# Kernel tuning notes

Hardware: AMD Instinct MI355X
Metric: run time of the kernel (lower is better)

Reference implementation:

```python
import jax, jax.numpy as jnp
import numpy as np

B, S, D, H, F = 8, 1024, 768, 12, 3072
DH = D // H
C_QUAD = 5.0
LN_EPS = 1e-5


def layer_norm(x, g, b):
    mu = jnp.mean(x, axis=-1, keepdims=True)
    var = jnp.mean(jnp.square(x - mu), axis=-1, keepdims=True)
    return (x - mu) * jax.lax.rsqrt(var + LN_EPS) * g + b


def setup_inputs() -> dict:
    key = jax.random.key(0)
    ks = jax.random.split(key, 8)
    s_in = 1.0 / np.sqrt(D)
    s_ff = 1.0 / np.sqrt(F)
    return {
        "x": jax.random.normal(ks[0], (B, S, D), jnp.float32),
        "wqkv": jax.random.normal(ks[1], (D, 3 * D), jnp.float32) * s_in,
        "bqkv": jnp.zeros((3 * D,), jnp.float32),
        "wo": jax.random.normal(ks[2], (D, D), jnp.float32) * s_in,
        "bo": jnp.zeros((D,), jnp.float32),
        "ln1_g": jnp.ones((D,), jnp.float32),
        "ln1_b": jnp.zeros((D,), jnp.float32),
        "w1": jax.random.normal(ks[3], (D, F), jnp.float32) * s_in,
        "b1": jnp.zeros((F,), jnp.float32),
        "w2": jax.random.normal(ks[4], (F, D), jnp.float32) * s_ff,
        "b2": jnp.zeros((D,), jnp.float32),
        "ln2_g": jnp.ones((D,), jnp.float32),
        "ln2_b": jnp.zeros((D,), jnp.float32),
    }


def quad2(scores):
    # Quad2 custom 'softmax': (s + c)^2 normalized by row sum
    s2 = jnp.square(scores + C_QUAD)
    return s2 / jnp.sum(s2, axis=-1, keepdims=True)


def reference(x, wqkv, bqkv, wo, bo, ln1_g, ln1_b, w1, b1, w2, b2, ln2_g, ln2_b):
    # --- pre-norm multi-head attention with Quad2 score normalization ---
    h = layer_norm(x, ln1_g, ln1_b)
    qkv = h @ wqkv + bqkv                              # [B,S,3D]
    q, k, v = jnp.split(qkv, 3, axis=-1)
    q = q.reshape(B, S, H, DH).transpose(0, 2, 1, 3)   # [B,H,S,Dh]
    k = k.reshape(B, S, H, DH).transpose(0, 2, 1, 3)
    v = v.reshape(B, S, H, DH).transpose(0, 2, 1, 3)
    scale = 1.0 / np.sqrt(DH)
    scores = jnp.einsum("bhqd,bhkd->bhqk", q, k) * scale
    attn = quad2(scores)                               # [B,H,S,S]
    ctx = jnp.einsum("bhqk,bhkd->bhqd", attn, v)
    ctx = ctx.transpose(0, 2, 1, 3).reshape(B, S, D)
    x = x + ctx @ wo + bo
    # --- pre-norm FFN ---
    h = layer_norm(x, ln2_g, ln2_b)
    h = jax.nn.gelu(h @ w1 + b1)
    x = x + h @ w2 + b2
    return x
```

## Files before the change

kernel.cpp:

```cpp
#include <hip/hip_runtime.h>
#include <hip/hip_bf16.h>

constexpr int B_ = 8;
constexpr int S_ = 1024;
constexpr int D_ = 768;
constexpr int H_ = 12;
constexpr int F_ = 3072;
constexpr int DH_ = 64;
constexpr int M_ = B_ * S_;
constexpr int PSZ = B_ * S_ * D_;

typedef __bf16 bf16x8 __attribute__((ext_vector_type(8)));
typedef float f32x4 __attribute__((ext_vector_type(4)));
typedef short s16x8 __attribute__((ext_vector_type(8)));
typedef short s16x4 __attribute__((ext_vector_type(4)));

__device__ __forceinline__ void gload_lds16(const __bf16* g, __bf16* l) {
    __builtin_amdgcn_global_load_lds(
        (const __attribute__((address_space(1))) void*)g,
        (__attribute__((address_space(3))) void*)l,
        16, 0, 0);
}

__device__ __forceinline__ float fast_gelu(float x) {
    float x3 = x * x * x;
    float z = 0.7978845608028654f * x + 0.035677408136300125f * x3;
    float e = __builtin_amdgcn_exp2f(-2.8853900817779268f * z);
    return x * __builtin_amdgcn_rcpf(1.0f + e);
}

__global__ __launch_bounds__(256) void transpose_cvt(const float* __restrict__ in,
                                                     __bf16* __restrict__ out,
                                                     int K, int N) {
    __shared__ float t[32][33];
    int tx = threadIdx.x, ty = threadIdx.y;
    int n0 = blockIdx.x * 32, k0 = blockIdx.y * 32;
#pragma unroll
    for (int i = 0; i < 4; ++i)
        t[ty + i * 8][tx] = in[(size_t)(k0 + ty + i * 8) * N + n0 + tx];
    __syncthreads();
#pragma unroll
    for (int i = 0; i < 4; ++i)
        out[(size_t)(n0 + ty + i * 8) * K + k0 + tx] = (__bf16)t[tx][ty + i * 8];
}

__global__ __launch_bounds__(256) void ln_kernel(const float* __restrict__ x,
                                                 const float* __restrict__ g,
                                                 const float* __restrict__ bb,
                                                 __bf16* __restrict__ out) {
    int row = blockIdx.x;
    const float* xr = x + (size_t)row * D_;
    int tid = threadIdx.x;
    float v[3];
    float s = 0.f, s2 = 0.f;
#pragma unroll
    for (int j = 0; j < 3; ++j) {
        v[j] = xr[tid + j * 256];
        s += v[j];
        s2 += v[j] * v[j];
    }
#pragma unroll
    for (int o = 32; o >= 1; o >>= 1) {
        s += __shfl_xor(s, o, 64);
        s2 += __shfl_xor(s2, o, 64);
    }
    __shared__ float red[8];
    int wid = tid >> 6, lane = tid & 63;
    if (lane == 0) { red[wid] = s; red[4 + wid] = s2; }
    __syncthreads();
    s = red[0] + red[1] + red[2] + red[3];
    s2 = red[4] + red[5] + red[6] + red[7];
    float mu = s * (1.0f / D_);
    float var = s2 * (1.0f / D_) - mu * mu;
    float rs = rsqrtf(var + 1e-5f);
    __bf16* orow = out + (size_t)row * D_;
#pragma unroll
    for (int j = 0; j < 3; ++j) {
        int i = tid + j * 256;
        orow[i] = (__bf16)((v[j] - mu) * rs * g[i] + bb[i]);
    }
}

template <int EPI>
__global__ __launch_bounds__(512) void gemmk(const __bf16* __restrict__ A,
                                             const __bf16* __restrict__ Bt,
                                             const float* __restrict__ bias,
                                             const float* __restrict__ res,
                                             float* __restrict__ outf,
                                             __bf16* __restrict__ outb,
                                             int M, int N, int K) {
    __shared__ __bf16 lds[2][16384];

    const int tid = threadIdx.x;
    const int lane = tid & 63, wid = tid >> 6;
    const int wm = wid >> 2, wn = wid & 3;
    const int gx = gridDim.x;
    const int nwg = gx * gridDim.y;
    int flat = blockIdx.y * gx + blockIdx.x;
    flat = (flat & 7) * (nwg >> 3) + (flat >> 3);
    const int bm = (flat / gx) * 128, bn = (flat % gx) * 128;
    const int l15 = lane & 15, l4 = lane >> 4;
    f32x4 acc[4][2] = {};

    const int r8 = tid >> 3;
    const int swc = ((tid & 7) ^ (r8 & 7)) * 8;
    const __bf16* ga = A + (size_t)(bm + r8) * K + swc;
    const __bf16* gb = Bt + (size_t)(bn + r8) * K + swc;
    const int NT = K / 64;

    auto stage = [&](int t, int s) {
        const int kt = t * 64;
        __bf16* base = &lds[s][0] + tid * 8;
        gload_lds16(ga + kt, base);
        gload_lds16(ga + kt + (size_t)64 * K, base + 4096);
        gload_lds16(gb + kt, base + 8192);
        gload_lds16(gb + kt + (size_t)64 * K, base + 12288);
    };

    stage(0, 0);
    for (int t = 0; t < NT; ++t) {
        if (t + 1 < NT) {
            stage(t + 1, (t + 1) & 1);
            asm volatile("s_waitcnt vmcnt(4)" ::: "memory");
        } else {
            asm volatile("s_waitcnt vmcnt(0)" ::: "memory");
        }
        asm volatile("s_barrier" ::: "memory");

        const __bf16* sA = &lds[t & 1][0];
        const __bf16* sB = sA + 8192;
        const int swr = (l15 & 7) * 8;
        bf16x8 a[4][2], b[2][2];
#pragma unroll
        for (int mf = 0; mf < 4; ++mf) {
            int row = wm * 64 + mf * 16 + l15;
#pragma unroll
            for (int ks = 0; ks < 2; ++ks)
                a[mf][ks] = *(const bf16x8*)&sA[row * 64 + ((ks * 32 + l4 * 8) ^ swr)];
        }
#pragma unroll
        for (int nf = 0; nf < 2; ++nf) {
            int row = wn * 32 + nf * 16 + l15;
#pragma unroll
            for (int ks = 0; ks < 2; ++ks)
                b[nf][ks] = *(const bf16x8*)&sB[row * 64 + ((ks * 32 + l4 * 8) ^ swr)];
        }
        asm volatile("s_waitcnt lgkmcnt(0)" ::: "memory");
        asm volatile("s_barrier" ::: "memory");
        __builtin_amdgcn_sched_barrier(0);

        __builtin_amdgcn_s_setprio(1);
#pragma unroll
        for (int ks = 0; ks < 2; ++ks)
#pragma unroll
            for (int mf = 0; mf < 4; ++mf)
#pragma unroll
                for (int nf = 0; nf < 2; ++nf)
                    acc[mf][nf] = __builtin_amdgcn_mfma_f32_16x16x32_bf16(
                        a[mf][ks], b[nf][ks], acc[mf][nf], 0, 0, 0);
        __builtin_amdgcn_s_setprio(0);
    }

    if constexpr (EPI == 0) {
#pragma unroll
        for (int nf = 0; nf < 2; ++nf) {
            int n = bn + wn * 32 + nf * 16 + l15;
            int part = n / 768;
            int n7 = n - part * 768;
            float bv = bias[n];
            size_t obase = (size_t)part * PSZ + (size_t)(n7 >> 6) * (S_ * DH_) + (n7 & 63);
#pragma unroll
            for (int mf = 0; mf < 4; ++mf) {
                int m0 = bm + wm * 64 + mf * 16 + l4 * 4;
                size_t rb = obase + (size_t)(m0 >> 10) * ((size_t)H_ * S_ * DH_) +
                            (size_t)(m0 & 1023) * DH_;
#pragma unroll
                for (int r = 0; r < 4; ++r)
                    outb[rb + (size_t)r * DH_] = (__bf16)(acc[mf][nf][r] + bv);
            }
        }
    } else {
#pragma unroll
        for (int mf = 0; mf < 4; ++mf) {
#pragma unroll
            for (int nf = 0; nf < 2; ++nf) {
#pragma unroll
                for (int r = 0; r < 4; ++r) {
                    int m = bm + wm * 64 + mf * 16 + l4 * 4 + r;
                    int n = bn + wn * 32 + nf * 16 + l15;
                    float val = acc[mf][nf][r] + bias[n];
                    if constexpr (EPI == 1) {
                        outf[(size_t)m * N + n] = val + res[(size_t)m * N + n];
                    } else {
                        outb[(size_t)m * N + n] = (__bf16)fast_gelu(val);
                    }
                }
            }
        }
    }
}

__global__ __launch_bounds__(256) void attn_kernel(const __bf16* __restrict__ qg,
                                                   const __bf16* __restrict__ kg,
                                                   const __bf16* __restrict__ vg,
                                                   __bf16* __restrict__ ctx) {
    __shared__ __bf16 Ks[64][72];
    __shared__ __bf16 Vt[64][72];
    __shared__ __bf16 Pw[4][32][72];
    __shared__ float den_l[4][32];
    int tid = threadIdx.x, lane = tid & 63, wid = tid >> 6;
    int l15 = lane & 15, l4 = lane >> 4;
    int bh = blockIdx.x >> 3, qt = blockIdx.x & 7;
    int q0 = qt * 128;
    const __bf16* qbase = qg + (size_t)bh * S_ * DH_;
    const __bf16* kbase = kg + (size_t)bh * S_ * DH_;
    const __bf16* vbase = vg + (size_t)bh * S_ * DH_;

    int wq0 = q0 + wid * 32;
    bf16x8 qf[2][2];
#pragma unroll
    for (int qi = 0; qi < 2; ++qi)
#pragma unroll
        for (int ks = 0; ks < 2; ++ks)
            qf[qi][ks] = *(const bf16x8*)(qbase + (size_t)(wq0 + qi * 16 + l15) * DH_ +
                                          ks * 32 + l4 * 8);

    f32x4 oacc[2][4] = {};
    float den[2] = {0.f, 0.f};
    const float scale = 0.125f;

    for (int k0 = 0; k0 < S_; k0 += 64) {
        {
            int key = tid >> 2, dc = (tid & 3) * 16;
            *(s16x8*)&Ks[key][dc] =
                *(const s16x8*)(kbase + (size_t)(k0 + key) * DH_ + dc);
            *(s16x8*)&Ks[key][dc + 8] =
                *(const s16x8*)(kbase + (size_t)(k0 + key) * DH_ + dc + 8);
            int vkey = tid & 63, dg = (tid >> 6) * 16;
            s16x8 v0 = *(const s16x8*)(vbase + (size_t)(k0 + vkey) * DH_ + dg);
            s16x8 v1 = *(const s16x8*)(vbase + (size_t)(k0 + vkey) * DH_ + dg + 8);
#pragma unroll
            for (int e = 0; e < 8; ++e) {
                Vt[dg + e][vkey] = ((const __bf16*)&v0)[e];
                Vt[dg + 8 + e][vkey] = ((const __bf16*)&v1)[e];
            }
        }
        __syncthreads();

        bf16x8 kf[4][2];
#pragma unroll
        for (int kfi = 0; kfi < 4; ++kfi)
#pragma unroll
            for (int ks = 0; ks < 2; ++ks)
                kf[kfi][ks] = *(const bf16x8*)&Ks[kfi * 16 + l15][ks * 32 + l4 * 8];

#pragma unroll
        for (int qi = 0; qi < 2; ++qi) {
#pragma unroll
            for (int kfi = 0; kfi < 4; ++kfi) {
                f32x4 sa = {};
                sa = __builtin_amdgcn_mfma_f32_16x16x32_bf16(kf[kfi][0], qf[qi][0], sa, 0, 0, 0);
                sa = __builtin_amdgcn_mfma_f32_16x16x32_bf16(kf[kfi][1], qf[qi][1], sa, 0, 0, 0);
                __bf16 pk[4];
#pragma unroll
                for (int r = 0; r < 4; ++r) {
                    float p = sa[r] * scale + 5.0f;
                    p = p * p;
                    den[qi] += p;
                    pk[r] = (__bf16)p;
                }
                *(s16x4*)&Pw[wid][qi * 16 + l15][kfi * 16 + l4 * 4] =
                    *(const s16x4*)pk;
            }
        }

#pragma unroll
        for (int mf = 0; mf < 2; ++mf) {
#pragma unroll
            for (int ks = 0; ks < 2; ++ks) {
                bf16x8 pa = *(const bf16x8*)&Pw[wid][mf * 16 + l15][ks * 32 + l4 * 8];
#pragma unroll
                for (int nf = 0; nf < 4; ++nf) {
                    bf16x8 vb = *(const bf16x8*)&Vt[nf * 16 + l15][ks * 32 + l4 * 8];
                    oacc[mf][nf] = __builtin_amdgcn_mfma_f32_16x16x32_bf16(
                        pa, vb, oacc[mf][nf], 0, 0, 0);
                }
            }
        }
        __syncthreads();
    }

#pragma unroll
    for (int qi = 0; qi < 2; ++qi) {
        den[qi] += __shfl_xor(den[qi], 16, 64);
        den[qi] += __shfl_xor(den[qi], 32, 64);
    }
    if (lane < 16) {
        den_l[wid][lane] = den[0];
        den_l[wid][16 + lane] = den[1];
    }
    __syncthreads();

    int b_ = bh / H_, h_ = bh - b_ * H_;
#pragma unroll
    for (int mf = 0; mf < 2; ++mf)
#pragma unroll
        for (int nf = 0; nf < 4; ++nf) {
#pragma unroll
            for (int r = 0; r < 4; ++r) {
                int qrow = mf * 16 + l4 * 4 + r;
                int dcol = nf * 16 + l15;
                float val = oacc[mf][nf][r] *
                            __builtin_amdgcn_rcpf(den_l[wid][qrow]);
                int sI = q0 + wid * 32 + qrow;
                ctx[((size_t)b_ * S_ + sI) * D_ + h_ * DH_ + dcol] = (__bf16)val;
            }
        }
}

extern "C" void kernel_launch(void* const* d_in, const int* in_sizes, int n_in,
                              void* d_out, int out_size, void* d_ws, size_t ws_size,
                              hipStream_t stream) {
    const float* x    = (const float*)d_in[0];
    const float* wqkv = (const float*)d_in[1];
    const float* bqkv = (const float*)d_in[2];
    const float* wo   = (const float*)d_in[3];
    const float* bo   = (const float*)d_in[4];
    const float* ln1g = (const float*)d_in[5];
    const float* ln1b = (const float*)d_in[6];
    const float* w1   = (const float*)d_in[7];
    const float* b1   = (const float*)d_in[8];
    const float* w2   = (const float*)d_in[9];
    const float* b2   = (const float*)d_in[10];
    const float* ln2g = (const float*)d_in[11];
    const float* ln2b = (const float*)d_in[12];
    float* out = (float*)d_out;

    char* ws = (char*)d_ws;
    size_t off = 0;
    auto alloc = [&](size_t bytes) {
        void* p = ws + off;
        off += (bytes + 255) & ~(size_t)255;
        return p;
    };
    __bf16* wqkvT = (__bf16*)alloc((size_t)(3 * D_) * D_ * 2);
    __bf16* woT   = (__bf16*)alloc((size_t)D_ * D_ * 2);
    __bf16* w1T   = (__bf16*)alloc((size_t)F_ * D_ * 2);
    __bf16* w2T   = (__bf16*)alloc((size_t)D_ * F_ * 2);
    float*  X2    = (float*)alloc((size_t)M_ * D_ * 4);
    __bf16* Hb    = (__bf16*)alloc((size_t)M_ * D_ * 2);
    __bf16* Q3    = (__bf16*)alloc((size_t)4 * PSZ * 2);
    __bf16* Kb = Q3 + (size_t)PSZ;
    __bf16* Vb = Q3 + (size_t)2 * PSZ;
    __bf16* Cx = Q3 + (size_t)3 * PSZ;

    transpose_cvt<<<dim3((3 * D_) / 32, D_ / 32), dim3(32, 8), 0, stream>>>(wqkv, wqkvT, D_, 3 * D_);
    transpose_cvt<<<dim3(D_ / 32, D_ / 32), dim3(32, 8), 0, stream>>>(wo, woT, D_, D_);
    transpose_cvt<<<dim3(F_ / 32, D_ / 32), dim3(32, 8), 0, stream>>>(w1, w1T, D_, F_);
    transpose_cvt<<<dim3(D_ / 32, F_ / 32), dim3(32, 8), 0, stream>>>(w2, w2T, F_, D_);

    ln_kernel<<<M_, 256, 0, stream>>>(x, ln1g, ln1b, Hb);
    gemmk<0><<<dim3((3 * D_) / 128, M_ / 128), 512, 0, stream>>>(
        Hb, wqkvT, bqkv, nullptr, nullptr, Q3, M_, 3 * D_, D_);
    attn_kernel<<<B_ * H_ * (S_ / 128), 256, 0, stream>>>(Q3, Kb, Vb, Cx);
    gemmk<1><<<dim3(D_ / 128, M_ / 128), 512, 0, stream>>>(
        Cx, woT, bo, x, X2, nullptr, M_, D_, D_);
    ln_kernel<<<M_, 256, 0, stream>>>(X2, ln2g, ln2b, Hb);
    gemmk<2><<<dim3(F_ / 128, M_ / 128), 512, 0, stream>>>(
        Hb, w1T, b1, nullptr, nullptr, Q3, M_, F_, D_);
    gemmk<1><<<dim3(D_ / 128, M_ / 128), 512, 0, stream>>>(
        Q3, w2T, b2, X2, out, nullptr, M_, D_, F_);
    (void)in_sizes; (void)n_in; (void)out_size; (void)ws_size;
}
```

Baseline: 221.3 us.

## Use 4-wave 64x64-per-wave GEMM for QKV/proj and XCD-aware attention block mapping

```diff
diff --git a/kernel.cpp b/kernel.cpp
--- a/kernel.cpp
+++ b/kernel.cpp
@@ -82,13 +82,134 @@
 }
 
 template <int EPI>
-__global__ __launch_bounds__(512) void gemmk(const __bf16* __restrict__ A,
-                                             const __bf16* __restrict__ Bt,
-                                             const float* __restrict__ bias,
-                                             const float* __restrict__ res,
-                                             float* __restrict__ outf,
-                                             __bf16* __restrict__ outb,
-                                             int M, int N, int K) {
+__device__ __forceinline__ void gemm4_body(const __bf16* __restrict__ A,
+                                           const __bf16* __restrict__ Bt,
+                                           const float* __restrict__ bias,
+                                           const float* __restrict__ res,
+                                           float* __restrict__ outf,
+                                           __bf16* __restrict__ outb,
+                                           int M, int N, int K) {
+    __shared__ __bf16 lds[2][16384];
+
+    const int tid = threadIdx.x;
+    const int lane = tid & 63, wid = tid >> 6;
+    const int wm = wid >> 1, wn = wid & 1;
+    const int gx = gridDim.x;
+    const int nwg = gx * gridDim.y;
+    int flat = blockIdx.y * gx + blockIdx.x;
+    flat = (flat & 7) * (nwg >> 3) + (flat >> 3);
+    const int bm = (flat / gx) * 128, bn = (flat % gx) * 128;
+    const int l15 = lane & 15, l4 = lane >> 4;
+    f32x4 acc[4][4] = {};
+
+    const int r8 = tid >> 3;
+    const int swc = ((tid & 7) ^ (r8 & 7)) * 8;
+    const __bf16* ga = A + (size_t)(bm + r8) * K + swc;
+    const __bf16* gb = Bt + (size_t)(bn + r8) * K + swc;
+    const int NT = K / 64;
+
+    auto stage = [&](int t, int s) {
+        const int kt = t * 64;
+        __bf16* base = &lds[s][0] + tid * 8;
+#pragma unroll
+        for (int j = 0; j < 4; ++j)
+            gload_lds16(ga + kt + (size_t)j * 32 * K, base + j * 2048);
+#pragma unroll
+        for (int j = 0; j < 4; ++j)
+            gload_lds16(gb + kt + (size_t)j * 32 * K, base + 8192 + j * 2048);
+    };
+
+    stage(0, 0);
+    for (int t = 0; t < NT; ++t) {
+        if (t + 1 < NT) {
+            stage(t + 1, (t + 1) & 1);
+            asm volatile("s_waitcnt vmcnt(8)" ::: "memory");
+        } else {
+            asm volatile("s_waitcnt vmcnt(0)" ::: "memory");
+        }
+        asm volatile("s_barrier" ::: "memory");
+
+        const __bf16* sA = &lds[t & 1][0];
+        const __bf16* sB = sA + 8192;
+        const int swr = (l15 & 7) * 8;
+        bf16x8 a[4][2], b[4][2];
+#pragma unroll
+        for (int mf = 0; mf < 4; ++mf) {
+            int row = wm * 64 + mf * 16 + l15;
+#pragma unroll
+            for (int ks = 0; ks < 2; ++ks)
+                a[mf][ks] = *(const bf16x8*)&sA[row * 64 + ((ks * 32 + l4 * 8) ^ swr)];
+        }
+#pragma unroll
+        for (int nf = 0; nf < 4; ++nf) {
+            int row = wn * 64 + nf * 16 + l15;
+#pragma unroll
+            for (int ks = 0; ks < 2; ++ks)
+                b[nf][ks] = *(const bf16x8*)&sB[row * 64 + ((ks * 32 + l4 * 8) ^ swr)];
+        }
+        asm volatile("s_waitcnt lgkmcnt(0)" ::: "memory");
+        asm volatile("s_barrier" ::: "memory");
+        __builtin_amdgcn_sched_barrier(0);
+
+        __builtin_amdgcn_s_setprio(1);
+#pragma unroll
+        for (int ks = 0; ks < 2; ++ks)
+#pragma unroll
+            for (int mf = 0; mf < 4; ++mf)
+#pragma unroll
+                for (int nf = 0; nf < 4; ++nf)
+                    acc[mf][nf] = __builtin_amdgcn_mfma_f32_16x16x32_bf16(
+                        a[mf][ks], b[nf][ks], acc[mf][nf], 0, 0, 0);
+        __builtin_amdgcn_s_setprio(0);
+    }
+
+    if constexpr (EPI == 0) {
+#pragma unroll
+        for (int nf = 0; nf < 4; ++nf) {
+            int n = bn + wn * 64 + nf * 16 + l15;
+            int part = n / 768;
+            int n7 = n - part * 768;
+            float bv = bias[n];
+            size_t obase = (size_t)part * PSZ + (size_t)(n7 >> 6) * (S_ * DH_) + (n7 & 63);
+#pragma unroll
+            for (int mf = 0; mf < 4; ++mf) {
+                int m0 = bm + wm * 64 + mf * 16 + l4 * 4;
+                size_t rb = obase + (size_t)(m0 >> 10) * ((size_t)H_ * S_ * DH_) +
+                            (size_t)(m0 & 1023) * DH_;
+#pragma unroll
+                for (int r = 0; r < 4; ++r)
+                    outb[rb + (size_t)r * DH_] = (__bf16)(acc[mf][nf][r] + bv);
+            }
+        }
+    } else {
+#pragma unroll
+        for (int mf = 0; mf < 4; ++mf) {
+#pragma unroll
+            for (int nf = 0; nf < 4; ++nf) {
+#pragma unroll
+                for (int r = 0; r < 4; ++r) {
+                    int m = bm + wm * 64 + mf * 16 + l4 * 4 + r;
+                    int n = bn + wn * 64 + nf * 16 + l15;
+                    float val = acc[mf][nf][r] + bias[n];
+                    if constexpr (EPI == 1) {
+                        outf[(size_t)m * N + n] = val + res[(size_t)m * N + n];
+                    } else {
+                        outb[(size_t)m * N + n] = (__bf16)fast_gelu(val);
+                    }
+                }
+            }
+        }
+    }
+}
+
+template <int EPI>
+__device__ __forceinline__ void gemmk_body(const __bf16* __restrict__ A,
+                                           const __bf16* __restrict__ Bt,
+                                           const float* __restrict__ bias,
+                                           const float* __restrict__ res,
+                                           float* __restrict__ outf,
+                                           __bf16* __restrict__ outb,
+                                           int M, int N, int K) {
     __shared__ __bf16 lds[2][16384];
 
     const int tid = threadIdx.x;
@@ -161,43 +282,43 @@
         __builtin_amdgcn_s_setprio(0);
     }
 
-    if constexpr (EPI == 0) {
+#pragma unroll
+    for (int mf = 0; mf < 4; ++mf) {
 #pragma unroll
         for (int nf = 0; nf < 2; ++nf) {
-            int n = bn + wn * 32 + nf * 16 + l15;
-            int part = n / 768;
-            int n7 = n - part * 768;
-            float bv = bias[n];
-            size_t obase = (size_t)part * PSZ + (size_t)(n7 >> 6) * (S_ * DH_) + (n7 & 63);
-#pragma unroll
-            for (int mf = 0; mf < 4; ++mf) {
-                int m0 = bm + wm * 64 + mf * 16 + l4 * 4;
-                size_t rb = obase + (size_t)(m0 >> 10) * ((size_t)H_ * S_ * DH_) +
-                            (size_t)(m0 & 1023) * DH_;
-#pragma unroll
-                for (int r = 0; r < 4; ++r)
-                    outb[rb + (size_t)r * DH_] = (__bf16)(acc[mf][nf][r] + bv);
-            }
-        }
-    } else {
-#pragma unroll
-        for (int mf = 0; mf < 4; ++mf) {
-#pragma unroll
-            for (int nf = 0; nf < 2; ++nf) {
-#pragma unroll
-                for (int r = 0; r < 4; ++r) {
-                    int m = bm + wm * 64 + mf * 16 + l4 * 4 + r;
-                    int n = bn + wn * 32 + nf * 16 + l15;
-                    float val = acc[mf][nf][r] + bias[n];
-                    if constexpr (EPI == 1) {
-                        outf[(size_t)m * N + n] = val + res[(size_t)m * N + n];
-                    } else {
-                        outb[(size_t)m * N + n] = (__bf16)fast_gelu(val);
-                    }
+#pragma unroll
+            for (int r = 0; r < 4; ++r) {
+                int m = bm + wm * 64 + mf * 16 + l4 * 4 + r;
+                int n = bn + wn * 32 + nf * 16 + l15;
+                float val = acc[mf][nf][r] + bias[n];
+                if constexpr (EPI == 1) {
+                    outf[(size_t)m * N + n] = val + res[(size_t)m * N + n];
+                } else {
+                    outb[(size_t)m * N + n] = (__bf16)fast_gelu(val);
                 }
             }
         }
     }
+    (void)outf;
+}
+
+__global__ __launch_bounds__(256) void g_qkv(const __bf16* A, const __bf16* Bt,
+                                             const float* bias, __bf16* outb) {
+    gemm4_body<0>(A, Bt, bias, nullptr, nullptr, outb, M_, 3 * D_, D_);
+}
+__global__ __launch_bounds__(256) void g_proj(const __bf16* A, const __bf16* Bt,
+                                              const float* bias, const float* res,
+                                              float* outf) {
+    gemm4_body<1>(A, Bt, bias, res, outf, nullptr, M_, D_, D_);
+}
+__global__ __launch_bounds__(512) void g_ffn1(const __bf16* A, const __bf16* Bt,
+                                              const float* bias, __bf16* outb) {
+    gemmk_body<2>(A, Bt, bias, nullptr, nullptr, outb, M_, F_, D_);
+}
+__global__ __launch_bounds__(512) void g_ffn2(const __bf16* A, const __bf16* Bt,
+                                              const float* bias, const float* res,
+                                              float* outf) {
+    gemmk_body<1>(A, Bt, bias, res, outf, nullptr, M_, D_, F_);
 }
 
 __global__ __launch_bounds__(256) void attn_kernel(const __bf16* __restrict__ qg,
@@ -210,7 +331,11 @@
     __shared__ float den_l[4][32];
     int tid = threadIdx.x, lane = tid & 63, wid = tid >> 6;
     int l15 = lane & 15, l4 = lane >> 4;
-    int bh = blockIdx.x >> 3, qt = blockIdx.x & 7;
+    int idx = blockIdx.x;
+    int xcd = idx & 7;
+    int c = idx >> 3;
+    int bh = xcd * 12 + (c >> 3);
+    int qt = c & 7;
     int q0 = qt * 128;
     const __bf16* qbase = qg + (size_t)bh * S_ * DH_;
     const __bf16* kbase = kg + (size_t)bh * S_ * DH_;
@@ -360,15 +485,11 @@
     transpose_cvt<<<dim3(D_ / 32, F_ / 32), dim3(32, 8), 0, stream>>>(w2, w2T, F_, D_);
 
     ln_kernel<<<M_, 256, 0, stream>>>(x, ln1g, ln1b, Hb);
-    gemmk<0><<<dim3((3 * D_) / 128, M_ / 128), 512, 0, stream>>>(
-        Hb, wqkvT, bqkv, nullptr, nullptr, Q3, M_, 3 * D_, D_);
+    g_qkv<<<dim3((3 * D_) / 128, M_ / 128), 256, 0, stream>>>(Hb, wqkvT, bqkv, Q3);
     attn_kernel<<<B_ * H_ * (S_ / 128), 256, 0, stream>>>(Q3, Kb, Vb, Cx);
-    gemmk<1><<<dim3(D_ / 128, M_ / 128), 512, 0, stream>>>(
-        Cx, woT, bo, x, X2, nullptr, M_, D_, D_);
+    g_proj<<<dim3(D_ / 128, M_ / 128), 256, 0, stream>>>(Cx, woT, bo, x, X2);
     ln_kernel<<<M_, 256, 0, stream>>>(X2, ln2g, ln2b, Hb);
-    gemmk<2><<<dim3(F_ / 128, M_ / 128), 512, 0, stream>>>(
-        Hb, w1T, b1, nullptr, nullptr, Q3, M_, F_, D_);
-    gemmk<1><<<dim3(D_ / 128, M_ / 128), 512, 0, stream>>>(
-        Q3, w2T, b2, X2, out, nullptr, M_, D_, F_);
+    g_ffn1<<<dim3(F_ / 128, M_ / 128), 512, 0, stream>>>(Hb, w1T, b1, Q3);
+    g_ffn2<<<dim3(D_ / 128, M_ / 128), 512, 0, stream>>>(Q3, w2T, b2, X2, out);
     (void)in_sizes; (void)n_in; (void)out_size; (void)ws_size;
 }
```

Result: slower. 226.1 us (+2.1%).
